# Performance work log

Hardware: AMD Instinct MI355X
Metric: run time of the kernel (lower is better)

The kernel has to match this reference:

```python
import jax, jax.numpy as jnp
import numpy as np

B, N, D, STK_TOTAL = 8, 2048, 128, 4000


def setup_inputs() -> dict:
    key = jax.random.key(0)
    k1, k2, k3, k4 = jax.random.split(key, 4)
    x = jax.random.normal(k1, (B, N, D), dtype=jnp.float32)
    stk_ten = jax.random.randint(k2, (B, N), 0, STK_TOTAL, dtype=jnp.int32)
    # learned parameter tables (trained state; original inits: ones / xavier-uniform)
    stk_matrix = jax.random.normal(k3, (STK_TOTAL, STK_TOTAL), dtype=jnp.float32)
    stk_weight = jax.random.normal(k4, (STK_TOTAL, STK_TOTAL), dtype=jnp.float32)
    return {"x": x, "stk_ten": stk_ten, "stk_matrix": stk_matrix, "stk_weight": stk_weight}


def reference(x, stk_ten, stk_matrix, stk_weight):
    # x: [B, N, D]; stk_ten: [B, N] int ids < STK_TOTAL
    idx = stk_ten.astype(jnp.int32)
    # per-batch double gather -> [B, N, N] submatrices (vectorized index_select x2)
    M = stk_matrix[idx[:, :, None], idx[:, None, :]]          # [B, N, N]
    W = jnp.abs(stk_weight[idx[:, :, None], idx[:, None, :]])  # [B, N, N]
    n = idx.shape[1]
    eye = jnp.eye(n, dtype=bool)                               # diag removal mask
    M = jnp.where(eye, jnp.float32(0.0), M)                    # stk_m_s - diag_embed(diag)
    W = jnp.where(eye, jnp.float32(0.0), W)
    # dropout is identity in inference mode (training=False)
    att = jax.nn.softmax(W, axis=2)                            # [B, N, N]
    out = jnp.matmul(M * att, x)                               # [B, N, D]
    return out
```

## Files before the change

### kernel.cpp

```cpp
#include <hip/hip_runtime.h>
#include <hip/hip_fp16.h>
#include <math.h>

#define BATCH 8
#define N 2048
#define D 128
#define ST 4000

#define TJ 64
#define IT 16
#define KQ 4
#define TPW 8

typedef short bf16x8 __attribute__((ext_vector_type(8)));
typedef float f32x4  __attribute__((ext_vector_type(4)));

__device__ __forceinline__ unsigned short f2bf(float f) {
    union { float f; unsigned u; } v; v.f = f;
    const unsigned r = v.u + 0x7FFFu + ((v.u >> 16) & 1u);
    return (unsigned short)(r >> 16);
}

__global__ __launch_bounds__(256) void pack_kernel(
    const float* __restrict__ M, const float* __restrict__ W,
    unsigned* __restrict__ P)
{
    const size_t i4 = ((size_t)blockIdx.x * 256 + threadIdx.x) * 4;
    const float4 m4 = *(const float4*)(M + i4);
    const float4 w4 = *(const float4*)(W + i4);
    uint4 o;
    o.x = ((unsigned)f2bf(m4.x) << 16) | (unsigned)__half_as_ushort(__float2half(fabsf(w4.x)));
    o.y = ((unsigned)f2bf(m4.y) << 16) | (unsigned)__half_as_ushort(__float2half(fabsf(w4.y)));
    o.z = ((unsigned)f2bf(m4.z) << 16) | (unsigned)__half_as_ushort(__float2half(fabsf(w4.z)));
    o.w = ((unsigned)f2bf(m4.w) << 16) | (unsigned)__half_as_ushort(__float2half(fabsf(w4.w)));
    *(uint4*)(P + i4) = o;
}

__global__ __launch_bounds__(1024) void sort_kernel(
    const int* __restrict__ stk_ten,
    int* __restrict__ sval,
    int* __restrict__ spos)
{
    __shared__ int hist[4000];
    __shared__ int base[4000];
    __shared__ int wsum[16];
    const int b = blockIdx.x, t = threadIdx.x;
    const int lane = t & 63, wv = t >> 6;
    const int* idxb = stk_ten + b * N;

    for (int j = t; j < 4000; j += 1024) hist[j] = 0;
    __syncthreads();
    const int v0 = idxb[t], v1 = idxb[t + 1024];
    atomicAdd(&hist[v0], 1);
    atomicAdd(&hist[v1], 1);
    __syncthreads();

    int h[4], c[4], run = 0;
    #pragma unroll
    for (int i = 0; i < 4; ++i) {
        const int bi = 4 * t + i;
        h[i] = (bi < 4000) ? hist[bi] : 0;
        run += h[i];
        c[i] = run;
    }
    const int tsum = run;
    int incl = tsum;
    #pragma unroll
    for (int d = 1; d < 64; d <<= 1) {
        const int tmp = __shfl_up(incl, d, 64);
        if (lane >= d) incl += tmp;
    }
    if (lane == 63) wsum[wv] = incl;
    __syncthreads();
    if (t < 16) {
        const int v = wsum[t];
        int iv = v;
        #pragma unroll
        for (int d = 1; d < 16; d <<= 1) {
            const int tmp = __shfl_up(iv, d, 64);
            if (lane >= d) iv += tmp;
        }
        wsum[t] = iv - v;
    }
    __syncthreads();
    const int ex = incl - tsum + wsum[wv];
    #pragma unroll
    for (int i = 0; i < 4; ++i) {
        const int bi = 4 * t + i;
        if (bi < 4000) base[bi] = ex + c[i] - h[i];
    }
    __syncthreads();
    for (int j = t; j < 4000; j += 1024) hist[j] = 0;
    __syncthreads();
    {
        const int p0 = base[v0] + atomicAdd(&hist[v0], 1);
        sval[b * N + p0] = v0; spos[b * N + p0] = t;
        const int p1 = base[v1] + atomicAdd(&hist[v1], 1);
        sval[b * N + p1] = v1; spos[b * N + p1] = t + 1024;
    }
}

__global__ __launch_bounds__(256) void xt_kernel(
    const float* __restrict__ x,
    const int* __restrict__ spos,
    unsigned short* __restrict__ xT)
{
    __shared__ float xs[TJ][129];
    __shared__ int sp_s[TJ];
    const int t  = threadIdx.x;
    const int b  = blockIdx.x >> 5;
    const int jt = blockIdx.x & 31;
    const int j0 = jt * TJ;
    if (t < TJ) sp_s[t] = spos[b * N + j0 + t];
    __syncthreads();
    const int tx = t & 31, ty = t >> 5;
    const float* xb = x + (size_t)b * N * D;
    #pragma unroll
    for (int p = 0; p < 8; ++p) {
        const int r = ty + 8 * p;
        const float* src = xb + (size_t)sp_s[r] * D;
        #pragma unroll
        for (int i = 0; i < 4; ++i)
            xs[r][tx + 32 * i] = src[tx + 32 * i];
    }
    __syncthreads();
    const int jp = t & 31, dd0 = t >> 5;
    unsigned short* xTb = xT + (size_t)b * D * N;
    #pragma unroll
    for (int q = 0; q < 16; ++q) {
        const int dd = dd0 + 8 * q;
        const unsigned lo = f2bf(xs[2 * jp][dd]);
        const unsigned hi = f2bf(xs[2 * jp + 1][dd]);
        *(unsigned*)(xTb + (size_t)dd * N + j0 + 2 * jp) = (hi << 16) | lo;
    }
}

__global__ __launch_bounds__(256, 2) void fused_kernel(
    const unsigned short* __restrict__ xT,
    const int* __restrict__ stk_ten,
    const unsigned* __restrict__ P,
    const int* __restrict__ sval,
    const int* __restrict__ spos,
    float* __restrict__ out)
{
    __shared__ __align__(16) unsigned short cs[KQ][IT * 72];
    __shared__ float accbuf[KQ][IT][136];
    __shared__ float lbuf[KQ][IT];
    __shared__ int ri_s[IT];

    const int t    = threadIdx.x;
    const int lane = t & 63;
    const int w    = t >> 6;
    const int b    = blockIdx.x >> 7;
    const int i0   = (blockIdx.x & 127) * IT;

    if (t < IT) ri_s[t] = stk_ten[b * N + i0 + t];
    __syncthreads();

    unsigned rowoff[IT];
    #pragma unroll
    for (int m = 0; m < IT; ++m) rowoff[m] = (unsigned)ri_s[m] * ST;

    const int* svb = sval + b * N;
    const int* spb = spos + b * N;
    const unsigned short* xTb = xT + (size_t)b * D * N;
    unsigned short* csw = &cs[w][0];

    f32x4 acc[8];
    #pragma unroll
    for (int nb = 0; nb < 8; ++nb)
        #pragma unroll
        for (int r = 0; r < 4; ++r) acc[nb][r] = 0.0f;
    float l_part[IT];
    #pragma unroll
    for (int m = 0; m < IT; ++m) l_part[m] = 0.0f;

    const int jbase = w * (TPW * TJ);
    const int brow  = lane & 15;
    const int bcol  = (lane >> 4) * 8;

    int cj = svb[jbase + lane];
    int pj = spb[jbase + lane];
    unsigned gv[IT];
    #pragma unroll
    for (int m = 0; m < IT; ++m) gv[m] = P[rowoff[m] + (unsigned)cj];

    for (int tt = 0; tt < TPW; ++tt) {
        const int j0  = jbase + tt * TJ;
        const int j0n = (tt == TPW - 1) ? jbase : j0 + TJ;

        const int cjn = svb[j0n + lane];
        const int pjn = spb[j0n + lane];
        uint4 bv[8];
        #pragma unroll
        for (int nb = 0; nb < 8; ++nb)
            bv[nb] = *(const uint4*)(xTb + (size_t)(nb * 16 + brow) * N + j0 + bcol);

        #pragma unroll
        for (int m = 0; m < IT; ++m) {
            const unsigned u = gv[m];
            const float mf = __uint_as_float(u & 0xFFFF0000u);
            const float wf = __half2float(__ushort_as_half((unsigned short)(u & 0xFFFFu)));
            const bool diag = (pj == i0 + m);
            const float e = diag ? 1.0f : __expf(wf);
            l_part[m] += e;
            const float c = diag ? 0.0f : mf * e;
            csw[m * 72 + lane] = f2bf(c);
        }

        const bf16x8 av0 = *(const bf16x8*)(csw + brow * 72 + bcol);
        const bf16x8 av1 = *(const bf16x8*)(csw + brow * 72 + 32 + bcol);

        unsigned gvn[IT];
        #pragma unroll
        for (int m = 0; m < IT; ++m) gvn[m] = P[rowoff[m] + (unsigned)cjn];

        #pragma unroll
        for (int nb = 0; nb < 8; ++nb)
            acc[nb] = __builtin_amdgcn_mfma_f32_16x16x32_bf16(
                av0, *(const bf16x8*)&bv[nb], acc[nb], 0, 0, 0);
        #pragma unroll
        for (int nb = 0; nb < 8; ++nb)
            bv[nb] = *(const uint4*)(xTb + (size_t)(nb * 16 + brow) * N + j0 + 32 + bcol);
        #pragma unroll
        for (int nb = 0; nb < 8; ++nb)
            acc[nb] = __builtin_amdgcn_mfma_f32_16x16x32_bf16(
                av1, *(const bf16x8*)&bv[nb], acc[nb], 0, 0, 0);

        #pragma unroll
        for (int m = 0; m < IT; ++m) gv[m] = gvn[m];
        cj = cjn; pj = pjn;
    }

    #pragma unroll
    for (int m = 0; m < IT; ++m) {
        float v = l_part[m];
        #pragma unroll
        for (int d = 1; d < 64; d <<= 1) v += __shfl_xor(v, d, 64);
        if (lane == 0) lbuf[w][m] = v;
    }
    #pragma unroll
    for (int nb = 0; nb < 8; ++nb)
        #pragma unroll
        for (int r = 0; r < 4; ++r)
            accbuf[w][(lane >> 4) * 4 + r][nb * 16 + (lane & 15)] = acc[nb][r];
    __syncthreads();

    #pragma unroll
    for (int rr = 0; rr < 4; ++rr) {
        const int row = 4 * w + rr;
        const float linv = 1.0f /
            (lbuf[0][row] + lbuf[1][row] + lbuf[2][row] + lbuf[3][row]);
        #pragma unroll
        for (int p = 0; p < 2; ++p) {
            const int dd = lane + 64 * p;
            const float s = accbuf[0][row][dd] + accbuf[1][row][dd] +
                            accbuf[2][row][dd] + accbuf[3][row][dd];
            out[((size_t)(b * N + i0 + row) << 7) + dd] = s * linv;
        }
    }
}

extern "C" void kernel_launch(void* const* d_in, const int* in_sizes, int n_in,
                              void* d_out, int out_size, void* d_ws, size_t ws_size,
                              hipStream_t stream) {
    const float* x          = (const float*)d_in[0];
    const int*   stk_ten    = (const int*)d_in[1];
    const float* stk_matrix = (const float*)d_in[2];
    const float* stk_weight = (const float*)d_in[3];
    float* out = (float*)d_out;

    unsigned* P = (unsigned*)d_ws;
    int* sval = (int*)(P + (size_t)ST * ST);
    int* spos = sval + BATCH * N;
    unsigned short* xT = (unsigned short*)(spos + BATCH * N);

    pack_kernel<<<(ST * ST) / 1024, 256, 0, stream>>>(stk_matrix, stk_weight, P);
    sort_kernel<<<BATCH, 1024, 0, stream>>>(stk_ten, sval, spos);
    xt_kernel<<<BATCH * (N / TJ), 256, 0, stream>>>(x, spos, xT);
    fused_kernel<<<BATCH * (N / IT), 256, 0, stream>>>(
        xT, stk_ten, P, sval, spos, out);
}
```

Baseline: 244.4 us.

## Precompute exp weights in pack kernel, shrink LDS, swizzle blocks, raise occupancy

The pack kernel now computes exp(|w|) once per table entry and stores m*exp(|w|) as bf16 alongside exp(|w|) as fp16. This removes the per-gathered-element exp and multiply from the fused kernel's inner loop. The per-wave accumulation buffers are merged into one shared tile reduced with LDS atomicAdd, which shrinks shared memory so the launch bound can be raised to 4 blocks per CU. Block indices are also remapped across the 8-way interleave so neighbouring batch rows land on the same XCD. Risks include fp16 range limits on exp(|w|), contention on the LDS atomics, and register spills at the higher occupancy target.

```diff
diff --git a/kernel.cpp b/kernel.cpp
--- a/kernel.cpp
+++ b/kernel.cpp
@@ -14,6 +14,7 @@
 
 typedef short bf16x8 __attribute__((ext_vector_type(8)));
 typedef float f32x4  __attribute__((ext_vector_type(4)));
+typedef unsigned u32x4 __attribute__((ext_vector_type(4)));
 
 __device__ __forceinline__ unsigned short f2bf(float f) {
     union { float f; unsigned u; } v; v.f = f;
@@ -26,14 +27,26 @@
     unsigned* __restrict__ P)
 {
     const size_t i4 = ((size_t)blockIdx.x * 256 + threadIdx.x) * 4;
-    const float4 m4 = *(const float4*)(M + i4);
-    const float4 w4 = *(const float4*)(W + i4);
-    uint4 o;
-    o.x = ((unsigned)f2bf(m4.x) << 16) | (unsigned)__half_as_ushort(__float2half(fabsf(w4.x)));
-    o.y = ((unsigned)f2bf(m4.y) << 16) | (unsigned)__half_as_ushort(__float2half(fabsf(w4.y)));
-    o.z = ((unsigned)f2bf(m4.z) << 16) | (unsigned)__half_as_ushort(__float2half(fabsf(w4.z)));
-    o.w = ((unsigned)f2bf(m4.w) << 16) | (unsigned)__half_as_ushort(__float2half(fabsf(w4.w)));
-    *(uint4*)(P + i4) = o;
+    const f32x4 m4 = __builtin_nontemporal_load((const f32x4*)(M + i4));
+    const f32x4 w4 = __builtin_nontemporal_load((const f32x4*)(W + i4));
+    u32x4 o;
+    {
+        const float e = __expf(fabsf(w4.x));
+        o.x = ((unsigned)f2bf(m4.x * e) << 16) | (unsigned)__half_as_ushort(__float2half(e));
+    }
+    {
+        const float e = __expf(fabsf(w4.y));
+        o.y = ((unsigned)f2bf(m4.y * e) << 16) | (unsigned)__half_as_ushort(__float2half(e));
+    }
+    {
+        const float e = __expf(fabsf(w4.z));
+        o.z = ((unsigned)f2bf(m4.z * e) << 16) | (unsigned)__half_as_ushort(__float2half(e));
+    }
+    {
+        const float e = __expf(fabsf(w4.w));
+        o.w = ((unsigned)f2bf(m4.w * e) << 16) | (unsigned)__half_as_ushort(__float2half(e));
+    }
+    *(u32x4*)(P + i4) = o;
 }
 
 __global__ __launch_bounds__(1024) void sort_kernel(
@@ -135,7 +148,7 @@
     }
 }
 
-__global__ __launch_bounds__(256, 2) void fused_kernel(
+__global__ __launch_bounds__(256, 4) void fused_kernel(
     const unsigned short* __restrict__ xT,
     const int* __restrict__ stk_ten,
     const unsigned* __restrict__ P,
@@ -144,17 +157,19 @@
     float* __restrict__ out)
 {
     __shared__ __align__(16) unsigned short cs[KQ][IT * 72];
-    __shared__ float accbuf[KQ][IT][136];
+    __shared__ float accs[IT][132];
     __shared__ float lbuf[KQ][IT];
     __shared__ int ri_s[IT];
 
     const int t    = threadIdx.x;
     const int lane = t & 63;
     const int w    = t >> 6;
-    const int b    = blockIdx.x >> 7;
-    const int i0   = (blockIdx.x & 127) * IT;
+    const int wg   = (blockIdx.x & 7) * 128 + (blockIdx.x >> 3);
+    const int b    = wg >> 7;
+    const int i0   = (wg & 127) * IT;
 
     if (t < IT) ri_s[t] = stk_ten[b * N + i0 + t];
+    for (int z = t; z < IT * 132; z += 256) (&accs[0][0])[z] = 0.0f;
     __syncthreads();
 
     unsigned rowoff[IT];
@@ -199,13 +214,10 @@
         #pragma unroll
         for (int m = 0; m < IT; ++m) {
             const unsigned u = gv[m];
-            const float mf = __uint_as_float(u & 0xFFFF0000u);
-            const float wf = __half2float(__ushort_as_half((unsigned short)(u & 0xFFFFu)));
+            const float e = __half2float(__ushort_as_half((unsigned short)(u & 0xFFFFu)));
             const bool diag = (pj == i0 + m);
-            const float e = diag ? 1.0f : __expf(wf);
-            l_part[m] += e;
-            const float c = diag ? 0.0f : mf * e;
-            csw[m * 72 + lane] = f2bf(c);
+            l_part[m] += diag ? 1.0f : e;
+            csw[m * 72 + lane] = diag ? (unsigned short)0 : (unsigned short)(u >> 16);
         }
 
         const bf16x8 av0 = *(const bf16x8*)(csw + brow * 72 + bcol);
@@ -243,7 +255,7 @@
     for (int nb = 0; nb < 8; ++nb)
         #pragma unroll
         for (int r = 0; r < 4; ++r)
-            accbuf[w][(lane >> 4) * 4 + r][nb * 16 + (lane & 15)] = acc[nb][r];
+            atomicAdd(&accs[(lane >> 4) * 4 + r][nb * 16 + (lane & 15)], acc[nb][r]);
     __syncthreads();
 
     #pragma unroll
@@ -254,9 +266,7 @@
         #pragma unroll
         for (int p = 0; p < 2; ++p) {
             const int dd = lane + 64 * p;
-            const float s = accbuf[0][row][dd] + accbuf[1][row][dd] +
-                            accbuf[2][row][dd] + accbuf[3][row][dd];
-            out[((size_t)(b * N + i0 + row) << 7) + dd] = s * linv;
+            out[((size_t)(b * N + i0 + row) << 7) + dd] = accs[row][dd] * linv;
         }
     }
 }
```

After: 275.1 us. 12.5% more time.
